# Optimization experiments

Hardware: AMD Instinct MI355X
Metric: run time of the kernel (lower is better)

The kernel has to match this reference:

```python
import jax, jax.numpy as jnp
import numpy as np

B, D, H, C = 8192, 1024, 128, 16


def setup_inputs() -> dict:
    key = jax.random.key(0)
    ks = jax.random.split(key, 6)
    x = jax.random.normal(ks[0], (B, D), dtype=jnp.float32)
    c = jax.random.randint(ks[1], (B,), 0, C, dtype=jnp.int32)
    # per-condition 2-layer MLP params (fc1: D->H, fc2: H->D), torch Linear layout [out,in]
    W1 = jax.random.normal(ks[2], (C, H, D), dtype=jnp.float32) * 0.02
    b1 = jax.random.normal(ks[3], (C, H), dtype=jnp.float32) * 0.02
    W2 = jax.random.normal(ks[4], (C, D, H), dtype=jnp.float32) * 0.02
    b2 = jax.random.normal(ks[5], (C, D), dtype=jnp.float32) * 0.02
    return {"x": x, "c": c, "W1": W1, "b1": b1, "W2": W2, "b2": b2}


def reference(x, c, W1, b1, W2, b2):
    # embeddingnet treated as identity: embedded_x = x  [B, D]
    # Hard condition routing: compute every condition's mini-MLP densely, then
    # select the row matching each sample's condition (jit-friendly grouped GEMM).
    h_all = jnp.einsum('bd,chd->cbh', x, W1) + b1[:, None, :]          # [C, B, H]
    out_all = jnp.einsum('cbh,cdh->cbd', h_all, W2) + b2[:, None, :]   # [C, B, D]
    masked = out_all[c, jnp.arange(x.shape[0])]                        # [B, D]
    # l2_embed = True branch
    norm = jnp.linalg.norm(masked, axis=1, keepdims=True) + 1e-10
    masked = masked / norm
    mask_norm = jnp.float32(0.0)
    embed_norm = jnp.linalg.norm(x)
    return (masked, mask_norm, embed_norm, x)
```

## Files before the change

### kernel.cpp

```cpp
#include <hip/hip_runtime.h>
#include <hip/hip_bf16.h>
#include <math.h>

#define B_ 8192
#define D_ 1024
#define H_ 128
#define C_ 16
#define BD (B_*D_)
#define SUBR 16
#define SLOTS 68
#define MAXSUB 150
#define GRID_F (8 * SLOTS)

using bf16x8 = __attribute__((ext_vector_type(8))) __bf16;
using f32x4  = __attribute__((ext_vector_type(4))) float;
typedef unsigned short ushort_t;


__device__ inline bf16x8 cvt8(float4 a, float4 b) {
    bf16x8 r;
    r[0] = (__bf16)a.x; r[1] = (__bf16)a.y; r[2] = (__bf16)a.z; r[3] = (__bf16)a.w;
    r[4] = (__bf16)b.x; r[5] = (__bf16)b.y; r[6] = (__bf16)b.z; r[7] = (__bf16)b.w;
    return r;
}
__device__ inline unsigned pack2(float a, float b) {
    unsigned ua = __builtin_bit_cast(unsigned short, (__bf16)a);
    unsigned ub = __builtin_bit_cast(unsigned short, (__bf16)b);
    return ua | (ub << 16);
}

__global__ __launch_bounds__(256) void k_prep(const float* __restrict__ W1f,
                                              const float* __restrict__ W2f,
                                              const int* __restrict__ c,
                                              const float* __restrict__ x,
                                              __bf16* __restrict__ w1s,
                                              __bf16* __restrict__ w2s,
                                              __bf16* __restrict__ xbf,
                                              int* __restrict__ w,
                                              float* __restrict__ xpart,
                                              float* __restrict__ out) {
    int bid = blockIdx.x, tid = threadIdx.x;
    if (bid < 128) {
#pragma unroll
        for (int u = 0; u < 8; ++u) {
            int g = bid * 2048 + u * 256 + tid;
            int cond = g >> 14, jf = (g >> 11) & 7, ks = (g >> 6) & 31, lam = g & 63;
            int l15 = lam & 15, kg = lam >> 4;
            const float* src = W1f + ((size_t)cond * 128 + jf * 16 + l15) * 1024 + ks * 32 + kg * 8;
            *(bf16x8*)(w1s + (size_t)g * 8) = cvt8(*(const float4*)src, *(const float4*)(src + 4));
        }
    } else if (bid < 256) {
        int wb = bid - 128;
#pragma unroll
        for (int u = 0; u < 8; ++u) {
            int g = wb * 2048 + u * 256 + tid;
            int cond = g >> 14, jf = (g >> 8) & 63, ks = (g >> 6) & 3, lam = g & 63;
            int l15 = lam & 15, kg = lam >> 4;
            const float* src = W2f + ((size_t)cond * 1024 + jf * 16 + l15) * 128 + ks * 32 + kg * 8;
            *(bf16x8*)(w2s + (size_t)g * 8) = cvt8(*(const float4*)src, *(const float4*)(src + 4));
        }
    } else if (bid == 256) {
        __shared__ int hist[C_], base[C_], poff[C_], nt[C_];
        if (tid < C_) hist[tid] = 0;
        __syncthreads();
        for (int i = tid; i < B_; i += 256) atomicAdd(&hist[c[i]], 1);
        __syncthreads();
        if (tid == 0) {
            int off = 0;
            for (int cc = 0; cc < C_; ++cc) {
                nt[cc] = (hist[cc] + SUBR - 1) >> 4;
                poff[cc] = off;
                base[cc] = off;
                off += nt[cc] * SUBR;
            }
        }
        __syncthreads();
        if (tid < C_) {
            int cc = tid, xcd = cc >> 1;
            int s0 = (cc & 1) ? nt[cc - 1] : 0;
            int end = poff[cc] + hist[cc];
            for (int t = 0; t < nt[cc]; ++t) {
                int* e = &w[32 + (xcd * MAXSUB + s0 + t) * 3];
                e[0] = cc; e[1] = poff[cc] + t * SUBR; e[2] = end;
            }
            if ((cc & 1) == 0) w[16 + xcd] = nt[cc] + nt[cc + 1];
        }
        __syncthreads();
        for (int i = tid; i < B_; i += 256) {
            int pos = atomicAdd(&base[c[i]], 1);
            w[8192 + pos] = i;
        }
    } else {
        int xb = bid - 257;
        size_t base0 = (size_t)xb * 16384;
        float xsq = 0.0f;
        float2* xo_base = (float2*)(out + (size_t)BD + 2);
#pragma unroll 4
        for (int u = 0; u < 8; ++u) {
            size_t idx = base0 + u * 2048 + tid * 8;
            float4 f0 = *(const float4*)(x + idx);
            float4 f1 = *(const float4*)(x + idx + 4);
            *(bf16x8*)(xbf + idx) = cvt8(f0, f1);
            float2* xo = xo_base + (idx >> 1);
            xo[0] = make_float2(f0.x, f0.y); xo[1] = make_float2(f0.z, f0.w);
            xo[2] = make_float2(f1.x, f1.y); xo[3] = make_float2(f1.z, f1.w);
            xsq += f0.x*f0.x + f0.y*f0.y + f0.z*f0.z + f0.w*f0.w
                 + f1.x*f1.x + f1.y*f1.y + f1.z*f1.z + f1.w*f1.w;
        }
        float s = xsq;
        s += __shfl_xor(s, 1);  s += __shfl_xor(s, 2);  s += __shfl_xor(s, 4);
        s += __shfl_xor(s, 8);  s += __shfl_xor(s, 16); s += __shfl_xor(s, 32);
        __shared__ float red[4];
        int lane = tid & 63, wv = tid >> 6;
        if (lane == 0) red[wv] = s;
        __syncthreads();
        if (tid == 0) xpart[xb] = red[0] + red[1] + red[2] + red[3];
    }
}

__global__ __launch_bounds__(512, 4) void k_f(const __bf16* __restrict__ xbf,
                                              const __bf16* __restrict__ w1s,
                                              const __bf16* __restrict__ w2s,
                                              const float* __restrict__ b1f,
                                              const float* __restrict__ b2f,
                                              const int* __restrict__ wsi,
                                              const float* __restrict__ xpart,
                                              float* __restrict__ out) {
    int xcd = blockIdx.x & 7, slot0 = blockIdx.x >> 3;
    int nsub = wsi[16 + xcd];
    const int* sidx = wsi + 8192;

    __shared__ ulong2 xot_raw[2048];
    __shared__ ushort_t Hs[16 * 128];
    __shared__ float sqs[16 * 8];
    char* ldsx = (char*)xot_raw;
    unsigned* Ot32 = (unsigned*)xot_raw;

    int tid = threadIdx.x, wv = tid >> 6, lane = tid & 63, l15 = lane & 15, kg = lane >> 4;
    int sr = wv * 2 + (lane >> 5);
    int cg = lane & 31;
    int skg = cg & 3, skb = cg >> 2;

    if (blockIdx.x == GRID_F - 1) {
        float v = xpart[tid];
        v += __shfl_xor(v, 1);  v += __shfl_xor(v, 2);  v += __shfl_xor(v, 4);
        v += __shfl_xor(v, 8);  v += __shfl_xor(v, 16); v += __shfl_xor(v, 32);
        if (lane == 0) sqs[wv] = v;
        __syncthreads();
        if (tid == 0) {
            float e = sqs[0] + sqs[1] + sqs[2] + sqs[3] + sqs[4] + sqs[5] + sqs[6] + sqs[7];
            out[BD] = 0.0f;
            out[BD + 1] = sqrtf(e);
        }
        __syncthreads();
    }

    for (int si = slot0; si < nsub; si += SLOTS) {
        const int* e = wsi + 32 + (xcd * MAXSUB + si) * 3;
        int cond = e[0], prow0 = e[1], end = e[2];

        {
            int pr = prow0 + sr;
            int orow = sidx[pr < end ? pr : (end - 1)];
            const char* xs = (const char*)xbf + (size_t)orow * 2048;
#pragma unroll
            for (int it = 0; it < 4; ++it) {
                int m = it * 32 + cg;
                bf16x8 v = *(const bf16x8*)(xs + m * 16);
                int ks = it * 8 + skb;
                *(bf16x8*)(ldsx + ks * 1024 + skg * 256 + ((sr ^ skb) * 16)) = v;
            }
        }
        __syncthreads();

        const char* bA = (const char*)w1s + (size_t)cond * 262144 + wv * 32768 + lane * 16;
        f32x4 acc = {};
#pragma unroll 1
        for (int kb = 0; kb < 4; ++kb) {
            bf16x8 b0 = *(const bf16x8*)(bA + (kb * 8 + 0) * 1024);
            bf16x8 b1 = *(const bf16x8*)(bA + (kb * 8 + 1) * 1024);
            bf16x8 b2 = *(const bf16x8*)(bA + (kb * 8 + 2) * 1024);
            bf16x8 b3 = *(const bf16x8*)(bA + (kb * 8 + 3) * 1024);
            bf16x8 b4 = *(const bf16x8*)(bA + (kb * 8 + 4) * 1024);
            bf16x8 b5 = *(const bf16x8*)(bA + (kb * 8 + 5) * 1024);
            bf16x8 b6 = *(const bf16x8*)(bA + (kb * 8 + 6) * 1024);
            bf16x8 b7 = *(const bf16x8*)(bA + (kb * 8 + 7) * 1024);
#pragma unroll
            for (int j = 0; j < 8; ++j) {
                int ks = kb * 8 + j;
                bf16x8 x0 = *(const bf16x8*)(ldsx + ks * 1024 + kg * 256 + ((l15 ^ (ks & 7)) * 16));
                bf16x8 bj = j == 0 ? b0 : j == 1 ? b1 : j == 2 ? b2 : j == 3 ? b3
                          : j == 4 ? b4 : j == 5 ? b5 : j == 6 ? b6 : b7;
                acc = __builtin_amdgcn_mfma_f32_16x16x32_bf16(x0, bj, acc, 0, 0, 0);
            }
        }
        __syncthreads();

        {
            int j0 = wv * 16 + l15;
            float bias = b1f[cond * 128 + j0];
            int sl0 = j0 >> 3, jb = j0 & 7;
#pragma unroll
            for (int v = 0; v < 4; ++v) {
                int r0 = kg * 4 + v;
                __bf16 h0 = (__bf16)(acc[v] + bias);
                Hs[r0 * 128 + ((sl0 ^ (r0 & 7)) * 8) + jb] = __builtin_bit_cast(ushort_t, h0);
            }
        }
        __syncthreads();

        bf16x8 pa[4];
#pragma unroll
        for (int i = 0; i < 4; ++i)
            pa[i] = *(const bf16x8*)(Hs + l15 * 128 + (((i * 4 + kg) ^ (l15 & 7)) * 8));

        const char* w2b = (const char*)w2s + (size_t)cond * 262144 + wv * 32768 + lane * 16;
        float sq[4] = {0.f, 0.f, 0.f, 0.f};
        unsigned cswz = (unsigned)((kg & 1) << 4);
#pragma unroll 1
        for (int f = 0; f < 8; ++f) {
            const char* wb = w2b + f * 4096;
            bf16x8 q0 = *(const bf16x8*)(wb);
            bf16x8 q1 = *(const bf16x8*)(wb + 1024);
            bf16x8 q2 = *(const bf16x8*)(wb + 2048);
            bf16x8 q3 = *(const bf16x8*)(wb + 3072);
            f32x4 c0 = {};
            c0 = __builtin_amdgcn_mfma_f32_16x16x32_bf16(pa[0], q0, c0, 0, 0, 0);
            c0 = __builtin_amdgcn_mfma_f32_16x16x32_bf16(pa[1], q1, c0, 0, 0, 0);
            c0 = __builtin_amdgcn_mfma_f32_16x16x32_bf16(pa[2], q2, c0, 0, 0, 0);
            c0 = __builtin_amdgcn_mfma_f32_16x16x32_bf16(pa[3], q3, c0, 0, 0, 0);
            int jg = (wv * 8 + f) * 16 + l15;
            float bias = b2f[cond * 1024 + jg];
            float t0 = c0[0] + bias, t1 = c0[1] + bias, t2 = c0[2] + bias, t3 = c0[3] + bias;
            sq[0] += t0*t0; sq[1] += t1*t1; sq[2] += t2*t2; sq[3] += t3*t3;
            unsigned jc = (unsigned)jg ^ cswz;
            Ot32[(kg * 2    ) * 1024 + jc] = pack2(t0, t1);
            Ot32[(kg * 2 + 1) * 1024 + jc] = pack2(t2, t3);
        }
#pragma unroll
        for (int v = 0; v < 4; ++v) {
            float s = sq[v];
            s += __shfl_xor(s, 1); s += __shfl_xor(s, 2);
            s += __shfl_xor(s, 4); s += __shfl_xor(s, 8);
            if (l15 == 0) sqs[(kg * 4 + v) * 8 + wv] = s;
        }
        __syncthreads();

#pragma unroll 1
        for (int rr = 0; rr < 2; ++rr) {
            int r = wv * 2 + rr;
            int pr = prow0 + r;
            if (pr < end) {
                int orow = sidx[pr];
                float s = sqs[r*8+0] + sqs[r*8+1] + sqs[r*8+2] + sqs[r*8+3]
                        + sqs[r*8+4] + sqs[r*8+5] + sqs[r*8+6] + sqs[r*8+7];
                float inv = 1.0f / (sqrtf(s) + 1e-10f);
                int hi = (r & 1) * 16;
                unsigned rswz = (unsigned)(((r >> 2) & 1) << 4);
                const unsigned* base = Ot32 + (r >> 1) * 1024;
                float4* go = (float4*)(out + (size_t)orow * D_);
#pragma unroll
                for (int it = 0; it < 4; ++it) {
                    unsigned cu = (unsigned)(lane * 4 + it * 256) ^ rswz;
                    uint4 u = *(const uint4*)(base + cu);
                    float4 v;
                    v.x = (float)__builtin_bit_cast(__bf16, (ushort_t)(u.x >> hi)) * inv;
                    v.y = (float)__builtin_bit_cast(__bf16, (ushort_t)(u.y >> hi)) * inv;
                    v.z = (float)__builtin_bit_cast(__bf16, (ushort_t)(u.z >> hi)) * inv;
                    v.w = (float)__builtin_bit_cast(__bf16, (ushort_t)(u.w >> hi)) * inv;
                    go[lane + it * 64] = v;
                }
            }
        }
        __syncthreads();
    }
}

extern "C" void kernel_launch(void* const* d_in, const int* in_sizes, int n_in,
                              void* d_out, int out_size, void* d_ws, size_t ws_size,
                              hipStream_t stream) {
    const float* x  = (const float*)d_in[0];
    const int*   c  = (const int*)d_in[1];
    const float* W1 = (const float*)d_in[2];
    const float* b1 = (const float*)d_in[3];
    const float* W2 = (const float*)d_in[4];
    const float* b2 = (const float*)d_in[5];
    float* out = (float*)d_out;
    char* ws = (char*)d_ws;
    int* wsi = (int*)ws;
    float* xpart = (float*)(ws + 131072);
    __bf16* w1s  = (__bf16*)(ws + 262144);
    __bf16* w2s  = (__bf16*)(ws + 4456448);
    __bf16* xbf  = (__bf16*)(ws + 8650752);

    k_prep<<<769, 256, 0, stream>>>(W1, W2, c, x, w1s, w2s, xbf, wsi, xpart, out);
    k_f<<<GRID_F, 512, 0, stream>>>(xbf, w1s, w2s, b1, b2, wsi, xpart, out);
}
```

Baseline: 66.03 us.

## Stage weight bf16 swizzle through LDS for coalesced loads; split x conversion blocks

The W1/W2 fp32-to-bf16 fragment reordering now reads contiguous global memory, writes into an XOR-swizzled LDS staging buffer, then writes the permuted fragment layout out contiguously. Previously each thread gathered scattered strided rows from global memory. The x conversion and copy work is also split across twice as many blocks, each doing half the work, with the partial-norm reduction extended to read 1024 partials. The cost is 32 KB of LDS and a barrier in the weight blocks, plus a larger prep grid.

```diff
diff --git a/kernel.cpp b/kernel.cpp
--- a/kernel.cpp
+++ b/kernel.cpp
@@ -39,25 +39,47 @@
                                               int* __restrict__ w,
                                               float* __restrict__ xpart,
                                               float* __restrict__ out) {
+    __shared__ ulong2 stg[2048];
+    bf16x8* stgv = (bf16x8*)stg;
     int bid = blockIdx.x, tid = threadIdx.x;
+
     if (bid < 128) {
+        size_t mbase = (size_t)bid * 2048;
 #pragma unroll
         for (int u = 0; u < 8; ++u) {
-            int g = bid * 2048 + u * 256 + tid;
-            int cond = g >> 14, jf = (g >> 11) & 7, ks = (g >> 6) & 31, lam = g & 63;
-            int l15 = lam & 15, kg = lam >> 4;
-            const float* src = W1f + ((size_t)cond * 128 + jf * 16 + l15) * 1024 + ks * 32 + kg * 8;
-            *(bf16x8*)(w1s + (size_t)g * 8) = cvt8(*(const float4*)src, *(const float4*)(src + 4));
+            int ml = u * 256 + tid;
+            const float* src = W1f + (mbase + ml) * 8;
+            float4 f0 = *(const float4*)src, f1 = *(const float4*)(src + 4);
+            int row = ml >> 7, cc8 = ml & 127;
+            stgv[row * 128 + (cc8 ^ (row & 7))] = cvt8(f0, f1);
+        }
+        __syncthreads();
+#pragma unroll
+        for (int u = 0; u < 8; ++u) {
+            int o = u * 256 + tid;
+            int ks = o >> 6, kg = (o >> 4) & 3, l15 = o & 15;
+            bf16x8 v = stgv[l15 * 128 + ((ks * 4 + kg) ^ (l15 & 7))];
+            *(bf16x8*)(w1s + (mbase + o) * 8) = v;
         }
     } else if (bid < 256) {
-        int wb = bid - 128;
+        int b = bid - 128;
+        size_t mbase = (size_t)b * 2048;
 #pragma unroll
         for (int u = 0; u < 8; ++u) {
-            int g = wb * 2048 + u * 256 + tid;
-            int cond = g >> 14, jf = (g >> 8) & 63, ks = (g >> 6) & 3, lam = g & 63;
-            int l15 = lam & 15, kg = lam >> 4;
-            const float* src = W2f + ((size_t)cond * 1024 + jf * 16 + l15) * 128 + ks * 32 + kg * 8;
-            *(bf16x8*)(w2s + (size_t)g * 8) = cvt8(*(const float4*)src, *(const float4*)(src + 4));
+            int ml = u * 256 + tid;
+            const float* src = W2f + (mbase + ml) * 8;
+            float4 f0 = *(const float4*)src, f1 = *(const float4*)(src + 4);
+            int rr = ml >> 4, cc8 = ml & 15;
+            stgv[rr * 16 + (cc8 ^ (rr & 15))] = cvt8(f0, f1);
+        }
+        __syncthreads();
+#pragma unroll
+        for (int u = 0; u < 8; ++u) {
+            int o = u * 256 + tid;
+            int jfr = o >> 8, ks = (o >> 6) & 3, kg = (o >> 4) & 3, l15 = o & 15;
+            int rr = jfr * 16 + l15, cc8 = ks * 4 + kg;
+            bf16x8 v = stgv[rr * 16 + (cc8 ^ (rr & 15))];
+            *(bf16x8*)(w2s + (mbase + o) * 8) = v;
         }
     } else if (bid == 256) {
         __shared__ int hist[C_], base[C_], poff[C_], nt[C_];
@@ -92,11 +114,11 @@
         }
     } else {
         int xb = bid - 257;
-        size_t base0 = (size_t)xb * 16384;
+        size_t base0 = (size_t)xb * 8192;
         float xsq = 0.0f;
         float2* xo_base = (float2*)(out + (size_t)BD + 2);
-#pragma unroll 4
-        for (int u = 0; u < 8; ++u) {
+#pragma unroll
+        for (int u = 0; u < 4; ++u) {
             size_t idx = base0 + u * 2048 + tid * 8;
             float4 f0 = *(const float4*)(x + idx);
             float4 f1 = *(const float4*)(x + idx + 4);
@@ -142,7 +164,7 @@
     int skg = cg & 3, skb = cg >> 2;
 
     if (blockIdx.x == GRID_F - 1) {
-        float v = xpart[tid];
+        float v = xpart[tid] + xpart[tid + 512];
         v += __shfl_xor(v, 1);  v += __shfl_xor(v, 2);  v += __shfl_xor(v, 4);
         v += __shfl_xor(v, 8);  v += __shfl_xor(v, 16); v += __shfl_xor(v, 32);
         if (lane == 0) sqs[wv] = v;
@@ -293,6 +315,6 @@
     __bf16* w2s  = (__bf16*)(ws + 4456448);
     __bf16* xbf  = (__bf16*)(ws + 8650752);
 
-    k_prep<<<769, 256, 0, stream>>>(W1, W2, c, x, w1s, w2s, xbf, wsi, xpart, out);
+    k_prep<<<1281, 256, 0, stream>>>(W1, W2, c, x, w1s, w2s, xbf, wsi, xpart, out);
     k_f<<<GRID_F, 512, 0, stream>>>(xbf, w1s, w2s, b1, b2, wsi, xpart, out);
 }
```

Measured after the change: 64.21 us. -2.8%, faster.
